# Performance work log

Hardware: AMD Instinct MI355X
Metric: run time of the kernel (lower is better)

Reference implementation:

```python
import jax, jax.numpy as jnp
import numpy as np

EPS = 1e-8       # module eps
LN_EPS = 1e-5    # torch LayerNorm default
TEMP = 1.0       # relevance_temperature
STRENGTH = 1.0   # reweight_strength default (None -> 1.0)

Q, W, A = 64, 16, 64
D, C, H = 512, 512, 512


def _ln(x, g, b):
    m = x.mean(-1, keepdims=True)
    v = ((x - m) ** 2).mean(-1, keepdims=True)
    return (x - m) / jnp.sqrt(v + LN_EPS) * g + b


def _mlp(x, g, b, w1, b1, w2, b2):
    # LayerNorm -> Linear -> GELU(exact) -> Linear
    h = jax.nn.gelu(_ln(x, g, b) @ w1 + b1, approximate=False)
    return h @ w2 + b2


def setup_inputs() -> dict:
    key = jax.random.key(0)
    ks = iter(jax.random.split(key, 40))
    s = 0.02

    def lin(din, dout):
        return (jax.random.normal(next(ks), (din, dout), jnp.float32) * s,
                jnp.zeros((dout,), jnp.float32))

    inp = {
        "query_atoms": jax.random.normal(next(ks), (Q, A, D), jnp.float32),
        "query_masses": jax.random.uniform(next(ks), (Q, A), jnp.float32, 0.01, 1.0),
        "class_atoms": jax.random.normal(next(ks), (W, A, D), jnp.float32),
        "class_masses": jax.random.uniform(next(ks), (W, A), jnp.float32, 0.01, 1.0),
        "class_summary": jax.random.normal(next(ks), (W, C), jnp.float32),
        "episode_context": jax.random.normal(next(ks), (W, C), jnp.float32),
    }
    # query_proj
    inp["qg"], inp["qb"] = jnp.ones((D,), jnp.float32), jnp.zeros((D,), jnp.float32)
    inp["qw1"], inp["qb1"] = lin(D, H)
    inp["qw2"], inp["qb2"] = lin(H, H)
    # atom_proj
    inp["ag"], inp["ab"] = jnp.ones((D,), jnp.float32), jnp.zeros((D,), jnp.float32)
    inp["aw1"], inp["ab1"] = lin(D, H)
    inp["aw2"], inp["ab2"] = lin(H, H)
    # context_proj (input 2*C)
    inp["cg"], inp["cb"] = jnp.ones((2 * C,), jnp.float32), jnp.zeros((2 * C,), jnp.float32)
    inp["cw1"], inp["cb1"] = lin(2 * C, H)
    inp["cw2"], inp["cb2"] = lin(H, H)
    # relevance_head (input 4*H, output 1)
    inp["rg"], inp["rb"] = jnp.ones((4 * H,), jnp.float32), jnp.zeros((4 * H,), jnp.float32)
    inp["rw1"], inp["rb1"] = lin(4 * H, H)
    inp["rw2"], inp["rb2"] = lin(H, 1)
    return inp


def reference(query_atoms, query_masses, class_atoms, class_masses,
              class_summary, episode_context,
              qg, qb, qw1, qb1, qw2, qb2,
              ag, ab, aw1, ab1, aw2, ab2,
              cg, cb, cw1, cb1, cw2, cb2,
              rg, rb, rw1, rb1, rw2, rb2):
    # normalize query masses, pool query atoms -> [Q, D]
    qm = jnp.maximum(query_masses, 0.0)
    qm = qm / jnp.maximum(qm.sum(-1, keepdims=True), EPS)
    pooled = jnp.einsum('qa,qad->qd', qm, query_atoms)

    qh = _mlp(pooled, qg, qb, qw1, qb1, qw2, qb2)            # [Q, H]
    ah = _mlp(class_atoms, ag, ab, aw1, ab1, aw2, ab2)       # [W, A, H]
    ch = _mlp(jnp.concatenate([class_summary, episode_context], -1),
              cg, cb, cw1, cb1, cw2, cb2)                    # [W, H]

    nq, (way, na, h) = qh.shape[0], ah.shape
    a4 = jnp.broadcast_to(ah[None], (nq, way, na, h))
    q4 = jnp.broadcast_to(qh[:, None, None, :], (nq, way, na, h))
    c4 = jnp.broadcast_to(ch[None, :, None, :], (nq, way, na, h))
    fused = jnp.concatenate([a4, q4, a4 * q4, jnp.abs(a4 - q4) + c4], -1)  # [Q,W,A,4H]

    relevance = _mlp(fused, rg, rb, rw1, rb1, rw2, rb2)[..., 0]  # [Q, W, A]

    combined = jnp.log(jnp.maximum(class_masses, EPS))[None] + relevance / TEMP
    rew = jax.nn.softmax(combined, axis=-1)
    mixed = (1.0 - STRENGTH) * class_masses[None] + STRENGTH * rew
    mixed = mixed / jnp.maximum(mixed.sum(-1, keepdims=True), EPS)
    entropy = -(mixed * jnp.log(jnp.maximum(mixed, EPS))).sum(-1)  # [Q, W]
    return mixed, entropy
```

## Files before the change

kernel.cpp:

```cpp
#include <hip/hip_runtime.h>


#define DEV static __device__ __forceinline__

typedef __attribute__((ext_vector_type(8))) __bf16 bf16x8;
typedef __attribute__((ext_vector_type(4))) float f32x4;
typedef unsigned short ushort_t;

DEV ushort_t f2bf(float f) {
  unsigned u = __builtin_bit_cast(unsigned, f);
  u = (u + 0x7fffu + ((u >> 16) & 1u)) >> 16;
  return (ushort_t)u;
}

DEV float gelu_fast(float x) {
  const float y = x * 0.70710678118654752f;
  const float z = fabsf(y);
  const float t = __fdividef(1.0f, 1.0f + 0.3275911f * z);
  float p = 1.061405429f;
  p = p * t - 1.453152027f;
  p = p * t + 1.421413741f;
  p = p * t - 0.284496736f;
  p = p * t + 0.254829592f;
  const float e = 1.0f - p * t * __expf(-z * z);
  const float erfv = copysignf(e, y);
  return 0.5f * x * (1.0f + erfv);
}

#define OFF_XQB    0
#define OFF_XAB    16384
#define OFF_XCB    278528
#define OFF_HAB    286720
#define OFF_HQB    548864
#define OFF_HCB    565248
#define OFF_AHH    569344
#define OFF_QH     1093632
#define OFF_S1     1126400
#define OFF_B1     1126912
#define OFF_WT2    1127424
#define OFF_RW1LOT 1389568
#define OFF_RW1MIT 1520640
#define OFF_AW1T   1651712
#define OFF_QW1T   1782784
#define OFF_CW1T   1913856
#define OFF_AW2T   2176000
#define OFF_QW2T   2307072
#define OFF_CW2T   2438144
#define OFF_YA     OFF_AW1T
#define OFF_YQ     OFF_AW2T
#define OFF_CHH    OFF_XCB
#define OFF_AHHS   OFF_XAB
#define OFF_QHS    OFF_XQB


DEV void transpose_tile(const float* __restrict__ src, int koff, int kt, int ct,
                        ushort_t* __restrict__ dst, int ldk, float* sh, int tid) {
  float (*t)[65] = (float(*)[65])sh;
  for (int idx = tid; idx < 4096; idx += 512) {
    const int r = idx >> 6, c = idx & 63;
    t[r][c] = src[(koff + kt + r) * 512 + ct + c];
  }
  __syncthreads();
  for (int idx = tid; idx < 4096; idx += 512) {
    const int c = idx >> 6, r = idx & 63;
    dst[(ct + c) * ldk + kt + r] = f2bf(t[r][c]);
  }
}

__global__ __launch_bounds__(512) void pre0_kernel(
    const float* __restrict__ qa, const float* __restrict__ qm,
    const float* __restrict__ ca, const float* __restrict__ csum,
    const float* __restrict__ ectx,
    const float* __restrict__ qg, const float* __restrict__ qb,
    const float* __restrict__ ag, const float* __restrict__ ab,
    const float* __restrict__ cg, const float* __restrict__ cb,
    const float* __restrict__ rw1, const float* __restrict__ rg,
    const float* __restrict__ rb,
    const float* __restrict__ aw1, const float* __restrict__ qw1,
    const float* __restrict__ cw1, const float* __restrict__ aw2,
    const float* __restrict__ qw2, const float* __restrict__ cw2,
    float* __restrict__ ws) {
  __shared__ float sh[4160];
  const int b = blockIdx.x, tid = threadIdx.x, l = tid & 63, wv = tid >> 6;

  if (b < 128) {
    ushort_t* WT = (ushort_t*)(ws + OFF_WT2);
    float (*t)[65] = (float(*)[65])sh;
    const int kt = (b >> 3) << 6;
    const int ct = (b & 7) << 6;
    for (int idx = tid; idx < 4096; idx += 512) {
      const int r = idx >> 6, c = idx & 63;
      t[r][c] = rg[1024 + kt + r] * rw1[(1024 + kt + r) * 512 + ct + c];
    }
    __syncthreads();
    for (int idx = tid; idx < 4096; idx += 512) {
      const int c = idx >> 6, r = idx & 63;
      const int n = ct + c, k2 = kt + r;
      WT[((k2 >> 5) << 14) + (n << 5) + (k2 & 31)] = f2bf(t[r][c]);
    }
  } else if (b < 192) {
    const int bb = b - 128;
    transpose_tile(rw1, 0, (bb >> 3) << 6, (bb & 7) << 6,
                   (ushort_t*)(ws + OFF_RW1LOT), 512, sh, tid);
  } else if (b < 256) {
    const int bb = b - 192;
    transpose_tile(rw1, 512, (bb >> 3) << 6, (bb & 7) << 6,
                   (ushort_t*)(ws + OFF_RW1MIT), 512, sh, tid);
  } else if (b < 320) {
    const int bb = b - 256;
    transpose_tile(aw1, 0, (bb >> 3) << 6, (bb & 7) << 6,
                   (ushort_t*)(ws + OFF_AW1T), 512, sh, tid);
  } else if (b < 384) {
    const int bb = b - 320;
    transpose_tile(qw1, 0, (bb >> 3) << 6, (bb & 7) << 6,
                   (ushort_t*)(ws + OFF_QW1T), 512, sh, tid);
  } else if (b < 512) {
    const int bb = b - 384;
    transpose_tile(cw1, 0, (bb >> 3) << 6, (bb & 7) << 6,
                   (ushort_t*)(ws + OFF_CW1T), 1024, sh, tid);
  } else if (b < 576) {
    const int bb = b - 512;
    transpose_tile(aw2, 0, (bb >> 3) << 6, (bb & 7) << 6,
                   (ushort_t*)(ws + OFF_AW2T), 512, sh, tid);
  } else if (b < 640) {
    const int bb = b - 576;
    transpose_tile(qw2, 0, (bb >> 3) << 6, (bb & 7) << 6,
                   (ushort_t*)(ws + OFF_QW2T), 512, sh, tid);
  } else if (b < 704) {
    const int bb = b - 640;
    transpose_tile(cw2, 0, (bb >> 3) << 6, (bb & 7) << 6,
                   (ushort_t*)(ws + OFF_CW2T), 512, sh, tid);
  } else if (b < 720) {
    const int kc = (b - 704) << 7;
    float s0 = 0.f, s1 = 0.f, b0 = 0.f, b1v = 0.f;
    for (int k = kc; k < kc + 128; k += 2) {
      const float wa = rw1[(k << 9) + tid];
      const float wb = rw1[((k + 1) << 9) + tid];
      s0 += rg[k] * wa; b0 += rb[k] * wa;
      s1 += rg[k + 1] * wb; b1v += rb[k + 1] * wb;
    }
    atomicAdd(ws + OFF_S1 + tid, s0 + s1);
    atomicAdd(ws + OFF_B1 + tid, b0 + b1v);
  } else if (b < 784) {
    const int q = b - 720;
    if (wv == 0) {
      float m = fmaxf(qm[(q << 6) + l], 0.f);
      sh[l] = m;
      float s = m;
#pragma unroll
      for (int off = 1; off < 64; off <<= 1) s += __shfl_xor(s, off);
      if (l == 0) sh[64] = 1.0f / fmaxf(s, 1e-8f);
    }
    __syncthreads();
    const float sinv = sh[64];
    const float* qaq = qa + (q << 15) + tid;
    float v0 = 0.f, v1 = 0.f, v2 = 0.f, v3 = 0.f;
#pragma unroll 4
    for (int a = 0; a < 64; a += 4) {
      v0 += sh[a] * qaq[a << 9];
      v1 += sh[a + 1] * qaq[(a + 1) << 9];
      v2 += sh[a + 2] * qaq[(a + 2) << 9];
      v3 += sh[a + 3] * qaq[(a + 3) << 9];
    }
    const float v = (v0 + v1 + v2 + v3) * sinv;
    float s = v, ss = v * v;
#pragma unroll
    for (int off = 1; off < 64; off <<= 1) {
      s += __shfl_xor(s, off); ss += __shfl_xor(ss, off);
    }
    if (l == 0) { sh[128 + wv] = s; sh[136 + wv] = ss; }
    __syncthreads();
    float st = 0.f, sst = 0.f;
#pragma unroll
    for (int i = 0; i < 8; ++i) { st += sh[128 + i]; sst += sh[136 + i]; }
    const float mu = st * (1.0f / 512.0f);
    const float rstd = rsqrtf(sst * (1.0f / 512.0f) - mu * mu + 1e-5f);
    ((ushort_t*)(ws + OFF_XQB))[(q << 9) + tid] =
        f2bf((v - mu) * rstd * qg[tid] + qb[tid]);
  } else if (b < 912) {
    const int row = ((b - 784) << 3) + wv;
    const float* crow = ca + (row << 9);
    float x[8];
    float s = 0.f, ss = 0.f;
#pragma unroll
    for (int i = 0; i < 8; ++i) {
      x[i] = crow[l + (i << 6)];
      s += x[i]; ss += x[i] * x[i];
    }
#pragma unroll
    for (int off = 1; off < 64; off <<= 1) {
      s += __shfl_xor(s, off); ss += __shfl_xor(ss, off);
    }
    const float mu = s * (1.0f / 512.0f);
    const float rstd = rsqrtf(ss * (1.0f / 512.0f) - mu * mu + 1e-5f);
    ushort_t* xab = (ushort_t*)(ws + OFF_XAB);
#pragma unroll
    for (int i = 0; i < 8; ++i) {
      const int k = l + (i << 6);
      xab[(row << 9) + k] = f2bf((x[i] - mu) * rstd * ag[k] + ab[k]);
    }
  } else {
    const int w = b - 912;
    const float v0 = csum[(w << 9) + tid];
    const float v1 = ectx[(w << 9) + tid];
    float s = v0 + v1, ss = v0 * v0 + v1 * v1;
#pragma unroll
    for (int off = 1; off < 64; off <<= 1) {
      s += __shfl_xor(s, off); ss += __shfl_xor(ss, off);
    }
    if (l == 0) { sh[wv] = s; sh[8 + wv] = ss; }
    __syncthreads();
    float st = 0.f, sst = 0.f;
#pragma unroll
    for (int i = 0; i < 8; ++i) { st += sh[i]; sst += sh[8 + i]; }
    const float mu = st * (1.0f / 1024.0f);
    const float rstd = rsqrtf(sst * (1.0f / 1024.0f) - mu * mu + 1e-5f);
    ushort_t* xcb = (ushort_t*)(ws + OFF_XCB);
    xcb[(w << 10) + tid] = f2bf((v0 - mu) * rstd * cg[tid] + cb[tid]);
    xcb[(w << 10) + 512 + tid] =
        f2bf((v1 - mu) * rstd * cg[512 + tid] + cb[512 + tid]);
  }
}

template <int PHASE>
__global__ __launch_bounds__(256) void gemm_kernel(
    float* __restrict__ ws, const float* __restrict__ ba,
    const float* __restrict__ bq, const float* __restrict__ bc,
    const float* __restrict__ rg) {
  const int b = blockIdx.x, tid = threadIdx.x;
  const int l = tid & 63, wv = tid >> 6;

  const ushort_t* A; const ushort_t* BT;
  float* outF = nullptr; ushort_t* outB = nullptr; ushort_t* outS = nullptr;
  const float* bias = nullptr; const float* scl = nullptr;
  int M, K, t;

  if (PHASE == 1) {
    if (b < 128) {
      A = (const ushort_t*)(ws + OFF_XAB); BT = (const ushort_t*)(ws + OFF_AW1T);
      M = 1024; K = 512; outB = (ushort_t*)(ws + OFF_HAB); bias = ba;
      t = (b << 2) + wv;
    } else if (b < 136) {
      A = (const ushort_t*)(ws + OFF_XQB); BT = (const ushort_t*)(ws + OFF_QW1T);
      M = 64; K = 512; outB = (ushort_t*)(ws + OFF_HQB); bias = bq;
      t = ((b - 128) << 2) + wv;
    } else {
      A = (const ushort_t*)(ws + OFF_XCB); BT = (const ushort_t*)(ws + OFF_CW1T);
      M = 16; K = 1024; outB = (ushort_t*)(ws + OFF_HCB); bias = bc;
      t = ((b - 136) << 2) + wv;
    }
  } else if (PHASE == 2) {
    if (b < 128) {
      A = (const ushort_t*)(ws + OFF_HAB); BT = (const ushort_t*)(ws + OFF_AW2T);
      M = 1024; K = 512; outF = ws + OFF_AHH;
      outS = (ushort_t*)(ws + OFF_AHHS); bias = ba; scl = rg;
      t = (b << 2) + wv;
    } else if (b < 136) {
      A = (const ushort_t*)(ws + OFF_HQB); BT = (const ushort_t*)(ws + OFF_QW2T);
      M = 64; K = 512; outF = ws + OFF_QH;
      outS = (ushort_t*)(ws + OFF_QHS); bias = bq; scl = rg + 512;
      t = ((b - 128) << 2) + wv;
    } else {
      A = (const ushort_t*)(ws + OFF_HCB); BT = (const ushort_t*)(ws + OFF_CW2T);
      M = 16; K = 512; outF = ws + OFF_CHH; bias = bc;
      t = ((b - 136) << 2) + wv;
    }
  } else {
    if (b < 128) {
      A = (const ushort_t*)(ws + OFF_AHHS); BT = (const ushort_t*)(ws + OFF_RW1LOT);
      M = 1024; K = 512; outF = ws + OFF_YA;
      t = (b << 2) + wv;
    } else {
      A = (const ushort_t*)(ws + OFF_QHS); BT = (const ushort_t*)(ws + OFF_RW1MIT);
      M = 64; K = 512; outF = ws + OFF_YQ;
      t = ((b - 128) << 2) + wv;
    }
  }

  const int rt = t >> 4, ct = t & 15;
  const int r0 = rt << 5, c0 = ct << 5;
  const int kh = (l >> 4) << 3;
  const ushort_t* ap[2];
  const ushort_t* bp[2];
#pragma unroll
  for (int fr = 0; fr < 2; ++fr) {
    int r = r0 + (fr << 4) + (l & 15);
    if (r > M - 1) r = M - 1;
    ap[fr] = A + r * K + kh;
  }
#pragma unroll
  for (int cf = 0; cf < 2; ++cf)
    bp[cf] = BT + (c0 + (cf << 4) + (l & 15)) * K + kh;

  f32x4 acc[2][2] = {};
  const int nst = K >> 5;
#pragma unroll 4
  for (int ks = 0; ks < nst; ++ks) {
    bf16x8 afr[2], bfr[2];
#pragma unroll
    for (int fr = 0; fr < 2; ++fr)
      afr[fr] = __builtin_bit_cast(bf16x8, *(const uint4*)(ap[fr] + (ks << 5)));
#pragma unroll
    for (int cf = 0; cf < 2; ++cf)
      bfr[cf] = __builtin_bit_cast(bf16x8, *(const uint4*)(bp[cf] + (ks << 5)));
#pragma unroll
    for (int fr = 0; fr < 2; ++fr)
#pragma unroll
      for (int cf = 0; cf < 2; ++cf)
        acc[fr][cf] = __builtin_amdgcn_mfma_f32_16x16x32_bf16(
            afr[fr], bfr[cf], acc[fr][cf], 0, 0, 0);
  }

  const int rsub = (l >> 4) << 2, cl = l & 15;
#pragma unroll
  for (int fr = 0; fr < 2; ++fr) {
#pragma unroll
    for (int cf = 0; cf < 2; ++cf) {
      const int col = c0 + (cf << 4) + cl;
#pragma unroll
      for (int j = 0; j < 4; ++j) {
        const int row = r0 + (fr << 4) + rsub + j;
        if (row < M) {
          float v = acc[fr][cf][j];
          if (PHASE == 1) {
            outB[(row << 9) + col] = f2bf(gelu_fast(v + bias[col]));
          } else if (PHASE == 2) {
            v += bias[col];
            outF[(row << 9) + col] = v;
            if (outS) outS[(row << 9) + col] = f2bf(v * scl[col]);
          } else {
            outF[(row << 9) + col] = v;
          }
        }
      }
    }
  }
}

__global__ __launch_bounds__(1024, 4) void main_kernel(
    const float* __restrict__ AH, const float* __restrict__ QH,
    const float* __restrict__ CH, const ushort_t* __restrict__ WT2,
    const float* __restrict__ Ya, const float* __restrict__ Yq,
    const float* __restrict__ S1, const float* __restrict__ B1,
    const float* __restrict__ rb1, const float* __restrict__ rw2,
    const float* __restrict__ rb2, const float* __restrict__ cmass,
    float* __restrict__ out) {
  extern __shared__ char smem_raw[];
  float* qs = (float*)smem_raw;
  float* cs = qs + 1024;
  float* s1_s = cs + 512;
  float* s2_s = s1_s + 128;
  float* rel_s = s2_s + 128;
  float* misc = rel_s + 128;
  uint4* apv = (uint4*)(smem_raw + 8192);

  const int tid = threadIdx.x;
  const int l = tid & 63;
  const int wv = tid >> 6;
  const int w = blockIdx.x & 15;
  const int q0 = (blockIdx.x >> 4) << 1;

  qs[tid] = QH[(q0 << 9) + tid];
  if (tid < 512) cs[tid] = CH[(w << 9) + tid];
  if (tid < 128) { s1_s[tid] = 0.f; s2_s[tid] = 0.f; rel_s[tid] = 0.f; }
  __syncthreads();

  const int p = wv >> 3;
  const int s = wv & 7;
  const int rloc = ((s & 3) << 4) + (l & 15);
  const float* arow = AH + (((w << 6) + rloc) << 9);
  const float* qsrc = qs + (p << 9);
  const int kh = (l >> 4) << 3;
  float s1a = 0.f, s2a = 0.f;

#define BUILD(C, B) do { \
    _Pragma("unroll") for (int i_ = 0; i_ < 2; ++i_) { \
      const int ksl_ = (s >> 2) + (i_ << 1); \
      const int kg_ = ((C) << 7) + (ksl_ << 5) + kh; \
      const int ka_ = kg_ & 511; \
      const float4 a0_ = *(const float4*)(arow + ka_); \
      const float4 a1_ = *(const float4*)(arow + ka_ + 4); \
      const float4 q0_ = *(const float4*)(qsrc + ka_); \
      const float4 q1_ = *(const float4*)(qsrc + ka_ + 4); \
      const float av_[8] = {a0_.x, a0_.y, a0_.z, a0_.w, a1_.x, a1_.y, a1_.z, a1_.w}; \
      const float qv_[8] = {q0_.x, q0_.y, q0_.z, q0_.w, q1_.x, q1_.y, q1_.z, q1_.w}; \
      float vv_[8]; \
      if ((C) < 4) { \
        _Pragma("unroll") for (int j_ = 0; j_ < 8; ++j_) { \
          const float aq_ = av_[j_] * qv_[j_]; \
          vv_[j_] = aq_; \
          s1a += av_[j_] + aq_; \
          s2a += av_[j_] * av_[j_] + aq_ * aq_; \
        } \
      } else { \
        const float4 c0_ = *(const float4*)(cs + ka_); \
        const float4 c1_ = *(const float4*)(cs + ka_ + 4); \
        const float cv_[8] = {c0_.x, c0_.y, c0_.z, c0_.w, c1_.x, c1_.y, c1_.z, c1_.w}; \
        _Pragma("unroll") for (int j_ = 0; j_ < 8; ++j_) { \
          const float dd_ = fabsf(av_[j_] - qv_[j_]) + cv_[j_]; \
          vv_[j_] = dd_; \
          s1a += dd_; \
          s2a += dd_ * dd_; \
        } \
      } \
      union { __bf16 bv[8]; uint4 u4; } pk_; \
      _Pragma("unroll") for (int j_ = 0; j_ < 8; ++j_) pk_.bv[j_] = (__bf16)vv_[j_]; \
      apv[((B) << 11) + (p << 10) + (ksl_ << 8) + ((s & 3) << 6) + l] = pk_.u4; \
    } } while (0)

  BUILD(0, 0);
  if ((wv & 7) == 0) {
    float sq = 0.f, sqq = 0.f;
#pragma unroll
    for (int it = 0; it < 8; ++it) {
      const float vq = qsrc[l + (it << 6)];
      sq += vq; sqq += vq * vq;
    }
#pragma unroll
    for (int off = 1; off < 64; off <<= 1) {
      sq += __shfl_xor(sq, off); sqq += __shfl_xor(sqq, off);
    }
    if (l == 0) { misc[(p << 1)] = sq; misc[(p << 1) + 1] = sqq; }
  }
  __syncthreads();

  f32x4 acc0[4][2] = {}, acc1[4][2] = {};
  const int ncb = (wv << 5) + (l & 15);
#pragma unroll
  for (int c = 0; c < 8; ++c) {
    if (c < 7) {
      BUILD(c + 1, (c + 1) & 1);
    } else {
      s1a += __shfl_xor(s1a, 16); s1a += __shfl_xor(s1a, 32);
      s2a += __shfl_xor(s2a, 16); s2a += __shfl_xor(s2a, 32);
      if ((l >> 4) == 0) {
        atomicAdd(&s1_s[(p << 6) + rloc], s1a);
        atomicAdd(&s2_s[(p << 6) + rloc], s2a);
      }
    }
    const uint4* cbuf = apv + ((c & 1) << 11);
#pragma unroll
    for (int ksl = 0; ksl < 4; ++ksl) {
      const int ks32 = (c << 2) + ksl;
      const bf16x8 bfr0 = __builtin_bit_cast(bf16x8,
          *(const uint4*)(WT2 + (ks32 << 14) + (ncb << 5) + kh));
      const bf16x8 bfr1 = __builtin_bit_cast(bf16x8,
          *(const uint4*)(WT2 + (ks32 << 14) + ((ncb + 16) << 5) + kh));
      bf16x8 afr[4];
#pragma unroll
      for (int fr = 0; fr < 4; ++fr)
        afr[fr] = __builtin_bit_cast(bf16x8, cbuf[(ksl << 8) + (fr << 6) + l]);
#pragma unroll
      for (int fr = 0; fr < 4; ++fr) {
        acc0[fr][0] = __builtin_amdgcn_mfma_f32_16x16x32_bf16(
            afr[fr], bfr0, acc0[fr][0], 0, 0, 0);
        acc0[fr][1] = __builtin_amdgcn_mfma_f32_16x16x32_bf16(
            afr[fr], bfr1, acc0[fr][1], 0, 0, 0);
      }
#pragma unroll
      for (int fr = 0; fr < 4; ++fr)
        afr[fr] = __builtin_bit_cast(bf16x8,
            cbuf[(1 << 10) + (ksl << 8) + (fr << 6) + l]);
#pragma unroll
      for (int fr = 0; fr < 4; ++fr) {
        acc1[fr][0] = __builtin_amdgcn_mfma_f32_16x16x32_bf16(
            afr[fr], bfr0, acc1[fr][0], 0, 0, 0);
        acc1[fr][1] = __builtin_amdgcn_mfma_f32_16x16x32_bf16(
            afr[fr], bfr1, acc1[fr][1], 0, 0, 0);
      }
    }
    __syncthreads();
  }
#undef BUILD

  if (tid < 128) {
    const int pp = tid >> 6;
    const float s1r = s1_s[tid] + misc[pp << 1];
    const float s2r = s2_s[tid] + misc[(pp << 1) + 1];
    const float mu = s1r * (1.0f / 2048.0f);
    const float rs = rsqrtf(s2r * (1.0f / 2048.0f) - mu * mu + 1e-5f);
    s1_s[tid] = mu;
    s2_s[tid] = rs;
  }
  __syncthreads();

  {
    float yqv0[2], yqv1[2], s1c[2], b1c[2], w2c[2];
#pragma unroll
    for (int cf = 0; cf < 2; ++cf) {
      const int n = ncb + (cf << 4);
      yqv0[cf] = Yq[(q0 << 9) + n];
      yqv1[cf] = Yq[((q0 + 1) << 9) + n];
      s1c[cf] = S1[n];
      b1c[cf] = B1[n] + rb1[n];
      w2c[cf] = rw2[n];
    }
    const float* yab = Ya + (w << 15) + ncb;
    const int rsub = (l >> 4) << 2;
#pragma unroll
    for (int fr = 0; fr < 4; ++fr) {
#pragma unroll
      for (int j = 0; j < 4; ++j) {
        const int r = (fr << 4) + rsub + j;
        const float ya0 = yab[(r << 9)];
        const float ya1 = yab[(r << 9) + 16];
        {
          const float mu = s1_s[r], rs = s2_s[r];
          float rp = gelu_fast(rs * (acc0[fr][0][j] + ya0 + yqv0[0] - mu * s1c[0]) + b1c[0]) * w2c[0]
                   + gelu_fast(rs * (acc0[fr][1][j] + ya1 + yqv0[1] - mu * s1c[1]) + b1c[1]) * w2c[1];
          rp += __shfl_xor(rp, 1); rp += __shfl_xor(rp, 2);
          rp += __shfl_xor(rp, 4); rp += __shfl_xor(rp, 8);
          if ((l & 15) == 0) atomicAdd(&rel_s[r], rp);
        }
        {
          const float mu = s1_s[64 + r], rs = s2_s[64 + r];
          float rp = gelu_fast(rs * (acc1[fr][0][j] + ya0 + yqv1[0] - mu * s1c[0]) + b1c[0]) * w2c[0]
                   + gelu_fast(rs * (acc1[fr][1][j] + ya1 + yqv1[1] - mu * s1c[1]) + b1c[1]) * w2c[1];
          rp += __shfl_xor(rp, 1); rp += __shfl_xor(rp, 2);
          rp += __shfl_xor(rp, 4); rp += __shfl_xor(rp, 8);
          if ((l & 15) == 0) atomicAdd(&rel_s[64 + r], rp);
        }
      }
    }
  }
  __syncthreads();

  if (tid < 128) {
    const int pp = tid >> 6, a = tid & 63;
    const int qw = ((q0 + pp) << 4) + w;
    const float relv = rel_s[(pp << 6) + a] + rb2[0];
    const float x = logf(fmaxf(cmass[(w << 6) + a], 1e-8f)) + relv;
    float m = x;
#pragma unroll
    for (int off = 1; off < 64; off <<= 1) m = fmaxf(m, __shfl_xor(m, off));
    const float pv = expf(x - m);
    float sv = pv;
#pragma unroll
    for (int off = 1; off < 64; off <<= 1) sv += __shfl_xor(sv, off);
    float mix = pv / fmaxf(sv, 1e-8f);
    float s2 = mix;
#pragma unroll
    for (int off = 1; off < 64; off <<= 1) s2 += __shfl_xor(s2, off);
    mix = mix / fmaxf(s2, 1e-8f);
    const float et = -mix * logf(fmaxf(mix, 1e-8f));
    float ent = et;
#pragma unroll
    for (int off = 1; off < 64; off <<= 1) ent += __shfl_xor(ent, off);
    out[(qw << 6) + a] = mix;
    if (a == 0) out[65536 + qw] = ent;
  }
}

extern "C" void kernel_launch(void* const* d_in, const int* in_sizes, int n_in,
                              void* d_out, int out_size, void* d_ws, size_t ws_size,
                              hipStream_t stream) {
  (void)in_sizes; (void)n_in; (void)out_size; (void)ws_size;
  const float* q_atoms = (const float*)d_in[0];
  const float* q_mass  = (const float*)d_in[1];
  const float* c_atoms = (const float*)d_in[2];
  const float* c_mass  = (const float*)d_in[3];
  const float* c_sum   = (const float*)d_in[4];
  const float* e_ctx   = (const float*)d_in[5];
  const float* qg  = (const float*)d_in[6];  const float* qb  = (const float*)d_in[7];
  const float* qw1 = (const float*)d_in[8];  const float* qb1 = (const float*)d_in[9];
  const float* qw2 = (const float*)d_in[10]; const float* qb2 = (const float*)d_in[11];
  const float* ag  = (const float*)d_in[12]; const float* ab  = (const float*)d_in[13];
  const float* aw1 = (const float*)d_in[14]; const float* ab1 = (const float*)d_in[15];
  const float* aw2 = (const float*)d_in[16]; const float* ab2 = (const float*)d_in[17];
  const float* cg  = (const float*)d_in[18]; const float* cb  = (const float*)d_in[19];
  const float* cw1 = (const float*)d_in[20]; const float* cb1 = (const float*)d_in[21];
  const float* cw2 = (const float*)d_in[22]; const float* cb2 = (const float*)d_in[23];
  const float* rg  = (const float*)d_in[24]; const float* rb  = (const float*)d_in[25];
  const float* rw1 = (const float*)d_in[26]; const float* rb1 = (const float*)d_in[27];
  const float* rw2 = (const float*)d_in[28]; const float* rb2 = (const float*)d_in[29];

  float* ws = (float*)d_ws;
  float* out = (float*)d_out;

  hipMemsetAsync(ws + OFF_S1, 0, 1024 * sizeof(float), stream);
  pre0_kernel<<<928, 512, 0, stream>>>(q_atoms, q_mass, c_atoms, c_sum, e_ctx,
                                       qg, qb, ag, ab, cg, cb, rw1, rg, rb,
                                       aw1, qw1, cw1, aw2, qw2, cw2, ws);
  gemm_kernel<1><<<140, 256, 0, stream>>>(ws, ab1, qb1, cb1, rg);
  gemm_kernel<2><<<140, 256, 0, stream>>>(ws, ab2, qb2, cb2, rg);
  gemm_kernel<3><<<136, 256, 0, stream>>>(ws, nullptr, nullptr, nullptr, rg);

  static const size_t MAIN_SMEM = 8192 + 65536;
  hipFuncSetAttribute((const void*)main_kernel,
                      hipFuncAttributeMaxDynamicSharedMemorySize, (int)MAIN_SMEM);
  main_kernel<<<512, 1024, MAIN_SMEM, stream>>>(
      ws + OFF_AHH, ws + OFF_QH, ws + OFF_CHH,
      (const ushort_t*)(ws + OFF_WT2), ws + OFF_YA, ws + OFF_YQ,
      ws + OFF_S1, ws + OFF_B1, rb1, rw2, rb2, c_mass, out);
}
```

Baseline: 184.7 us.

## Halve main kernel block to 512 threads with 64-column warp tiles

```diff
diff --git a/kernel.cpp b/kernel.cpp
--- a/kernel.cpp
+++ b/kernel.cpp
@@ -337,7 +337,7 @@
   }
 }
 
-__global__ __launch_bounds__(1024, 4) void main_kernel(
+__global__ __launch_bounds__(512, 2) void main_kernel(
     const float* __restrict__ AH, const float* __restrict__ QH,
     const float* __restrict__ CH, const ushort_t* __restrict__ WT2,
     const float* __restrict__ Ya, const float* __restrict__ Yq,
@@ -361,21 +361,21 @@
   const int q0 = (blockIdx.x >> 4) << 1;
 
   qs[tid] = QH[(q0 << 9) + tid];
-  if (tid < 512) cs[tid] = CH[(w << 9) + tid];
+  qs[tid + 512] = QH[(q0 << 9) + 512 + tid];
+  cs[tid] = CH[(w << 9) + tid];
   if (tid < 128) { s1_s[tid] = 0.f; s2_s[tid] = 0.f; rel_s[tid] = 0.f; }
   __syncthreads();
 
-  const int p = wv >> 3;
-  const int s = wv & 7;
-  const int rloc = ((s & 3) << 4) + (l & 15);
+  const int p = wv >> 2;
+  const int s = wv & 3;
+  const int rloc = (s << 4) + (l & 15);
   const float* arow = AH + (((w << 6) + rloc) << 9);
   const float* qsrc = qs + (p << 9);
   const int kh = (l >> 4) << 3;
   float s1a = 0.f, s2a = 0.f;
 
 #define BUILD(C, B) do { \
-    _Pragma("unroll") for (int i_ = 0; i_ < 2; ++i_) { \
-      const int ksl_ = (s >> 2) + (i_ << 1); \
+    _Pragma("unroll") for (int ksl_ = 0; ksl_ < 4; ++ksl_) { \
       const int kg_ = ((C) << 7) + (ksl_ << 5) + kh; \
       const int ka_ = kg_ & 511; \
       const float4 a0_ = *(const float4*)(arow + ka_); \
@@ -405,11 +405,11 @@
       } \
       union { __bf16 bv[8]; uint4 u4; } pk_; \
       _Pragma("unroll") for (int j_ = 0; j_ < 8; ++j_) pk_.bv[j_] = (__bf16)vv_[j_]; \
-      apv[((B) << 11) + (p << 10) + (ksl_ << 8) + ((s & 3) << 6) + l] = pk_.u4; \
+      apv[((B) << 11) + (p << 10) + (ksl_ << 8) + (s << 6) + l] = pk_.u4; \
     } } while (0)
 
   BUILD(0, 0);
-  if ((wv & 7) == 0) {
+  if ((wv & 3) == 0) {
     float sq = 0.f, sqq = 0.f;
 #pragma unroll
     for (int it = 0; it < 8; ++it) {
@@ -424,8 +424,8 @@
   }
   __syncthreads();
 
-  f32x4 acc0[4][2] = {}, acc1[4][2] = {};
-  const int ncb = (wv << 5) + (l & 15);
+  f32x4 acc0[4][4] = {}, acc1[4][4] = {};
+  const int ncb = (wv << 6) + (l & 15);
 #pragma unroll
   for (int c = 0; c < 8; ++c) {
     if (c < 7) {
@@ -442,31 +442,28 @@
 #pragma unroll
     for (int ksl = 0; ksl < 4; ++ksl) {
       const int ks32 = (c << 2) + ksl;
-      const bf16x8 bfr0 = __builtin_bit_cast(bf16x8,
-          *(const uint4*)(WT2 + (ks32 << 14) + (ncb << 5) + kh));
-      const bf16x8 bfr1 = __builtin_bit_cast(bf16x8,
-          *(const uint4*)(WT2 + (ks32 << 14) + ((ncb + 16) << 5) + kh));
-      bf16x8 afr[4];
-#pragma unroll
-      for (int fr = 0; fr < 4; ++fr)
-        afr[fr] = __builtin_bit_cast(bf16x8, cbuf[(ksl << 8) + (fr << 6) + l]);
+      bf16x8 bfr[4];
+#pragma unroll
+      for (int cf = 0; cf < 4; ++cf)
+        bfr[cf] = __builtin_bit_cast(bf16x8,
+            *(const uint4*)(WT2 + (ks32 << 14) + ((ncb + (cf << 4)) << 5) + kh));
+      bf16x8 afr;
 #pragma unroll
       for (int fr = 0; fr < 4; ++fr) {
-        acc0[fr][0] = __builtin_amdgcn_mfma_f32_16x16x32_bf16(
-            afr[fr], bfr0, acc0[fr][0], 0, 0, 0);
-        acc0[fr][1] = __builtin_amdgcn_mfma_f32_16x16x32_bf16(
-            afr[fr], bfr1, acc0[fr][1], 0, 0, 0);
+        afr = __builtin_bit_cast(bf16x8, cbuf[(ksl << 8) + (fr << 6) + l]);
+#pragma unroll
+        for (int cf = 0; cf < 4; ++cf)
+          acc0[fr][cf] = __builtin_amdgcn_mfma_f32_16x16x32_bf16(
+              afr, bfr[cf], acc0[fr][cf], 0, 0, 0);
       }
 #pragma unroll
-      for (int fr = 0; fr < 4; ++fr)
-        afr[fr] = __builtin_bit_cast(bf16x8,
+      for (int fr = 0; fr < 4; ++fr) {
+        afr = __builtin_bit_cast(bf16x8,
             cbuf[(1 << 10) + (ksl << 8) + (fr << 6) + l]);
 #pragma unroll
-      for (int fr = 0; fr < 4; ++fr) {
-        acc1[fr][0] = __builtin_amdgcn_mfma_f32_16x16x32_bf16(
-            afr[fr], bfr0, acc1[fr][0], 0, 0, 0);
-        acc1[fr][1] = __builtin_amdgcn_mfma_f32_16x16x32_bf16(
-            afr[fr], bfr1, acc1[fr][1], 0, 0, 0);
+        for (int cf = 0; cf < 4; ++cf)
+          acc1[fr][cf] = __builtin_amdgcn_mfma_f32_16x16x32_bf16(
+              afr, bfr[cf], acc1[fr][cf], 0, 0, 0);
       }
     }
     __syncthreads();
@@ -485,9 +482,9 @@
   __syncthreads();
 
   {
-    float yqv0[2], yqv1[2], s1c[2], b1c[2], w2c[2];
-#pragma unroll
-    for (int cf = 0; cf < 2; ++cf) {
+    float yqv0[4], yqv1[4], s1c[4], b1c[4], w2c[4];
+#pragma unroll
+    for (int cf = 0; cf < 4; ++cf) {
       const int n = ncb + (cf << 4);
       yqv0[cf] = Yq[(q0 << 9) + n];
       yqv1[cf] = Yq[((q0 + 1) << 9) + n];
@@ -502,23 +499,22 @@
 #pragma unroll
       for (int j = 0; j < 4; ++j) {
         const int r = (fr << 4) + rsub + j;
-        const float ya0 = yab[(r << 9)];
-        const float ya1 = yab[(r << 9) + 16];
-        {
-          const float mu = s1_s[r], rs = s2_s[r];
-          float rp = gelu_fast(rs * (acc0[fr][0][j] + ya0 + yqv0[0] - mu * s1c[0]) + b1c[0]) * w2c[0]
-                   + gelu_fast(rs * (acc0[fr][1][j] + ya1 + yqv0[1] - mu * s1c[1]) + b1c[1]) * w2c[1];
-          rp += __shfl_xor(rp, 1); rp += __shfl_xor(rp, 2);
-          rp += __shfl_xor(rp, 4); rp += __shfl_xor(rp, 8);
-          if ((l & 15) == 0) atomicAdd(&rel_s[r], rp);
+        const float mu0 = s1_s[r], rs0 = s2_s[r];
+        const float mu1 = s1_s[64 + r], rs1 = s2_s[64 + r];
+        float rp0 = 0.f, rp1 = 0.f;
+#pragma unroll
+        for (int cf = 0; cf < 4; ++cf) {
+          const float ya = yab[(r << 9) + (cf << 4)];
+          rp0 += gelu_fast(rs0 * (acc0[fr][cf][j] + ya + yqv0[cf] - mu0 * s1c[cf]) + b1c[cf]) * w2c[cf];
+          rp1 += gelu_fast(rs1 * (acc1[fr][cf][j] + ya + yqv1[cf] - mu1 * s1c[cf]) + b1c[cf]) * w2c[cf];
         }
-        {
-          const float mu = s1_s[64 + r], rs = s2_s[64 + r];
-          float rp = gelu_fast(rs * (acc1[fr][0][j] + ya0 + yqv1[0] - mu * s1c[0]) + b1c[0]) * w2c[0]
-                   + gelu_fast(rs * (acc1[fr][1][j] + ya1 + yqv1[1] - mu * s1c[1]) + b1c[1]) * w2c[1];
-          rp += __shfl_xor(rp, 1); rp += __shfl_xor(rp, 2);
-          rp += __shfl_xor(rp, 4); rp += __shfl_xor(rp, 8);
-          if ((l & 15) == 0) atomicAdd(&rel_s[64 + r], rp);
+        rp0 += __shfl_xor(rp0, 1); rp0 += __shfl_xor(rp0, 2);
+        rp0 += __shfl_xor(rp0, 4); rp0 += __shfl_xor(rp0, 8);
+        rp1 += __shfl_xor(rp1, 1); rp1 += __shfl_xor(rp1, 2);
+        rp1 += __shfl_xor(rp1, 4); rp1 += __shfl_xor(rp1, 8);
+        if ((l & 15) == 0) {
+          atomicAdd(&rel_s[r], rp0);
+          atomicAdd(&rel_s[64 + r], rp1);
         }
       }
     }
@@ -588,7 +584,7 @@
   static const size_t MAIN_SMEM = 8192 + 65536;
   hipFuncSetAttribute((const void*)main_kernel,
                       hipFuncAttributeMaxDynamicSharedMemorySize, (int)MAIN_SMEM);
-  main_kernel<<<512, 1024, MAIN_SMEM, stream>>>(
+  main_kernel<<<512, 512, MAIN_SMEM, stream>>>(
       ws + OFF_AHH, ws + OFF_QH, ws + OFF_CHH,
       (const ushort_t*)(ws + OFF_WT2), ws + OFF_YA, ws + OFF_YQ,
       ws + OFF_S1, ws + OFF_B1, rb1, rw2, rb2, c_mass, out);
```

Result: faster. 179.5 us (-2.8%).
